# Optimization experiments

Hardware: AMD Instinct MI355X
Metric: run time of the kernel (lower is better)

Reference implementation:

```python
import jax, jax.numpy as jnp
import numpy as np

B, NQ, C = 2, 16384, 768
NH, NL, NP = 6, 1, 4
HW = 128
D = C // NH  # 128, deform_ratio = 1.0
EPS = 1e-6


def layernorm(x, g, b):
    m = jnp.mean(x, -1, keepdims=True)
    v = jnp.var(x, -1, keepdims=True)
    return (x - m) * jax.lax.rsqrt(v + EPS) * g + b


def setup_inputs() -> dict:
    key = jax.random.key(0)
    ks = jax.random.split(key, 16)
    n = lambda k, s, sc=1.0: jax.random.normal(k, s, jnp.float32) * sc
    return {
        "query": n(ks[0], (B, NQ, C)),
        "reference_points": jax.random.uniform(ks[1], (B, NQ, NL, 2), jnp.float32),
        "feat": n(ks[2], (B, NQ, C)),
        "spatial_shapes": jnp.array([[HW, HW]], jnp.int32),
        "level_start_index": jnp.array([0], jnp.int32),
        "qn_g": jnp.ones((C,), jnp.float32), "qn_b": jnp.zeros((C,), jnp.float32),
        "fn_g": jnp.ones((C,), jnp.float32), "fn_b": jnp.zeros((C,), jnp.float32),
        "gamma": n(ks[3], (C,), 0.1),
        "W_off": n(ks[4], (C, NH * NL * NP * 2), 0.02), "b_off": n(ks[5], (NH * NL * NP * 2,), 0.5),
        "W_attn": n(ks[6], (C, NH * NL * NP), 0.02), "b_attn": jnp.zeros((NH * NL * NP,), jnp.float32),
        "W_val": n(ks[7], (C, NH * D), 0.02), "b_val": jnp.zeros((NH * D,), jnp.float32),
        "W_out": n(ks[8], (NH * D, C), 0.02), "b_out": jnp.zeros((C,), jnp.float32),
    }


def _ms_deform_attn(q, rp, f, W_off, b_off, W_attn, b_attn, W_val, b_val, W_out, b_out, shapes, starts):
    Bq, Nq, _ = q.shape
    value = (f @ W_val + b_val).reshape(Bq, -1, NH, D)  # (B, Lin, H, D)
    off = (q @ W_off + b_off).reshape(Bq, Nq, NH, NL, NP, 2)
    aw = jax.nn.softmax((q @ W_attn + b_attn).reshape(Bq, Nq, NH, NL * NP), -1)
    aw = aw.reshape(Bq, Nq, NH, NL, NP)
    shapes_f = jnp.asarray(shapes, q.dtype)
    normalizer = jnp.stack([shapes_f[:, 1], shapes_f[:, 0]], -1)  # (NL, 2) = (W, H)
    loc = rp[:, :, None, :, None, :] + off / normalizer[None, None, None, :, None, :]
    out = jnp.zeros((Bq, Nq, NH, D), q.dtype)
    b_idx = jnp.arange(Bq)[:, None, None, None]
    h_idx = jnp.arange(NH)[None, None, :, None]
    for l in range(NL):
        Hl, Wl = int(shapes[l, 0]), int(shapes[l, 1])
        s = int(starts[l])
        v = value[:, s:s + Hl * Wl].reshape(Bq, Hl, Wl, NH, D)
        ll = loc[:, :, :, l]                        # (B, Nq, H, P, 2)
        # grid_sample bilinear, align_corners=False, zero padding
        x = ll[..., 0] * Wl - 0.5
        y = ll[..., 1] * Hl - 0.5
        x0 = jnp.floor(x); y0 = jnp.floor(y)
        x1 = x0 + 1.0;     y1 = y0 + 1.0
        wx1 = x - x0; wx0 = 1.0 - wx1
        wy1 = y - y0; wy0 = 1.0 - wy1
        def corner(xi, yi, w):
            valid = (xi >= 0) & (xi <= Wl - 1) & (yi >= 0) & (yi <= Hl - 1)
            xc = jnp.clip(xi, 0, Wl - 1).astype(jnp.int32)
            yc = jnp.clip(yi, 0, Hl - 1).astype(jnp.int32)
            g = v[b_idx, yc, xc, h_idx]             # (B, Nq, H, P, D)
            return g * (w * valid)[..., None]
        samp = (corner(x0, y0, wx0 * wy0) + corner(x1, y0, wx1 * wy0)
                + corner(x0, y1, wx0 * wy1) + corner(x1, y1, wx1 * wy1))
        out = out + jnp.einsum('bqhpd,bqhp->bqhd', samp, aw[:, :, :, l])
    return out.reshape(Bq, Nq, NH * D) @ W_out + b_out


def reference(query, reference_points, feat, spatial_shapes, level_start_index,
              qn_g, qn_b, fn_g, fn_b, gamma,
              W_off, b_off, W_attn, b_attn, W_val, b_val, W_out, b_out):
    shapes = np.asarray(spatial_shapes)
    starts = np.asarray(level_start_index)
    q = layernorm(query, qn_g, qn_b)
    f = layernorm(feat, fn_g, fn_b)
    attn = _ms_deform_attn(q, reference_points, f, W_off, b_off, W_attn, b_attn,
                           W_val, b_val, W_out, b_out, shapes, starts)
    return query + gamma * attn
```

## Files before the change

### kernel.cpp

```cpp
#include <hip/hip_runtime.h>
#include <stdint.h>

typedef unsigned short u16;
typedef float f32x4 __attribute__((ext_vector_type(4)));
typedef short s16x8 __attribute__((ext_vector_type(8)));

#define K_DIM 768
#define M_ROWS 32768
#define NQ_ 16384
#define HW_ 128

__device__ __forceinline__ float bf2f(u16 u) {
    union { uint32_t u; float f; } c; c.u = ((uint32_t)u) << 16; return c.f;
}
__device__ __forceinline__ u16 f2bf(float f) {
    union { float f; uint32_t u; } c; c.f = f;
    uint32_t u = c.u;
    u += 0x7FFFu + ((u >> 16) & 1);
    return (u16)(u >> 16);
}

__device__ __forceinline__ void gload_lds16(const void* g, void* l) {
    __builtin_amdgcn_global_load_lds((const __attribute__((address_space(1))) void*)g,
                                     (__attribute__((address_space(3))) void*)l, 16, 0, 0);
}

__global__ void prep_all_kernel(const float* __restrict__ Wval, const float* __restrict__ Wout,
                                const float* __restrict__ Woff, const float* __restrict__ Wattn,
                                const float* __restrict__ boff, const float* __restrict__ battn,
                                u16* __restrict__ wv_t, u16* __restrict__ wo_t,
                                u16* __restrict__ woa_t, float* __restrict__ bias) {
    int idx = blockIdx.x * 256 + threadIdx.x;
    const int SZ = 768 * K_DIM;
    if (idx < SZ) {
        int n = idx / K_DIM, k = idx - n * K_DIM;
        wv_t[idx] = f2bf(Wval[(size_t)k * 768 + n]);
    } else if (idx < 2 * SZ) {
        int r = idx - SZ;
        int n = r / K_DIM, k = r - n * K_DIM;
        wo_t[r] = f2bf(Wout[(size_t)k * 768 + n]);
    } else if (idx < 2 * SZ + 128 * K_DIM) {
        int r = idx - 2 * SZ;
        int n = r / K_DIM, k = r - n * K_DIM;
        float v = 0.0f;
        if (n < 48)      v = Woff[(size_t)k * 48 + n];
        else if (n < 72) v = Wattn[(size_t)k * 24 + (n - 48)];
        woa_t[r] = f2bf(v);
        if (r < 128) bias[r] = r < 48 ? boff[r] : (r < 72 ? battn[r - 48] : 0.0f);
    }
}

__global__ __launch_bounds__(192) void ln_kernel(const float* __restrict__ x,
                                                 const float* __restrict__ g,
                                                 const float* __restrict__ b,
                                                 u16* __restrict__ out) {
    int row = blockIdx.x;
    int tid = threadIdx.x;
    const float4 v = ((const float4*)(x + (size_t)row * K_DIM))[tid];
    float s  = v.x + v.y + v.z + v.w;
    float s2 = v.x * v.x + v.y * v.y + v.z * v.z + v.w * v.w;
#pragma unroll
    for (int off = 32; off >= 1; off >>= 1) {
        s  += __shfl_down(s, off);
        s2 += __shfl_down(s2, off);
    }
    __shared__ float red[6];
    int wv = tid >> 6, lane = tid & 63;
    if (lane == 0) { red[wv] = s; red[3 + wv] = s2; }
    __syncthreads();
    s  = red[0] + red[1] + red[2];
    s2 = red[3] + red[4] + red[5];
    float mean = s * (1.0f / K_DIM);
    float var  = s2 * (1.0f / K_DIM) - mean * mean;
    float inv  = rsqrtf(var + 1e-6f);
    const float4 gg = ((const float4*)g)[tid];
    const float4 bb = ((const float4*)b)[tid];
    ushort4 o;
    o.x = f2bf((v.x - mean) * inv * gg.x + bb.x);
    o.y = f2bf((v.y - mean) * inv * gg.y + bb.y);
    o.z = f2bf((v.z - mean) * inv * gg.z + bb.z);
    o.w = f2bf((v.w - mean) * inv * gg.w + bb.w);
    ((ushort4*)(out + (size_t)row * K_DIM))[tid] = o;
}

#define EP_BF16 0
#define EP_F32 1
#define EP_FINAL 2

template <int EP, int NX, int BN = 128>
__global__ __launch_bounds__(512) void gemm_kernel(
        const u16* __restrict__ A, const u16* __restrict__ Bt,
        const float* __restrict__ bias, void* __restrict__ out, int ld_out,
        const float* __restrict__ query, const float* __restrict__ gamma) {
    constexpr int NF = BN / 64;
    constexpr int BCH = BN / 64;
    constexpr int BUF = 16384 + BN * 128;
    constexpr int NWG = NX * (M_ROWS / 128);
    constexpr int CPX = NWG / 8;
    __shared__ __align__(16) char smem[2 * BUF];
    const int lane = threadIdx.x & 63;
    const int wv = threadIdx.x >> 6;
    const int wr = wv >> 2, wc = wv & 3;
    const int lr = lane & 15, lg = lane >> 4;
    const int wg  = blockIdx.x;
    const int swz = (wg & 7) * CPX + (wg >> 3);
    const int m0 = (swz / NX) * 128;
    const int n0 = (swz % NX) * BN;

    f32x4 acc[4][NF] = {};

    const u16* Ab = A + (size_t)m0 * K_DIM;
    const u16* Bb = Bt + (size_t)n0 * K_DIM;

    auto stage = [&](char* buf, int kt) {
#pragma unroll
        for (int c = 0; c < 2; ++c) {
            int chunk = wv * 2 + c;
            int row = chunk * 8 + (lane >> 3);
            int slot = (lane & 7) ^ (row & 7);
            gload_lds16(Ab + (size_t)row * K_DIM + kt + slot * 8, buf + chunk * 1024);
        }
#pragma unroll
        for (int c = 0; c < BCH; ++c) {
            int chunk = wv * BCH + c;
            int row = chunk * 8 + (lane >> 3);
            int slot = (lane & 7) ^ (row & 7);
            gload_lds16(Bb + (size_t)row * K_DIM + kt + slot * 8, buf + 16384 + chunk * 1024);
        }
    };

    stage(smem, 0);
    asm volatile("s_waitcnt vmcnt(0)" ::: "memory");
    __builtin_amdgcn_s_barrier();
    __builtin_amdgcn_sched_barrier(0);

    constexpr int NT = K_DIM / 64;
    int cur = 0;
#pragma unroll 2
    for (int t = 0; t < NT; ++t) {
        const char* rb = smem + cur * BUF;
        if (t + 1 < NT) stage(smem + (cur ^ 1) * BUF, (t + 1) * 64);
#pragma unroll
        for (int kk = 0; kk < 2; ++kk) {
            s16x8 af[4], bfr[NF];
#pragma unroll
            for (int m = 0; m < 4; ++m) {
                int row = wr * 64 + m * 16 + lr;
                int slot = (kk * 4 + lg) ^ (row & 7);
                af[m] = *(const s16x8*)(rb + row * 128 + slot * 16);
            }
#pragma unroll
            for (int n = 0; n < NF; ++n) {
                int row = wc * (BN / 4) + n * 16 + lr;
                int slot = (kk * 4 + lg) ^ (row & 7);
                bfr[n] = *(const s16x8*)(rb + 16384 + row * 128 + slot * 16);
            }
            __builtin_amdgcn_s_setprio(1);
#pragma unroll
            for (int m = 0; m < 4; ++m)
#pragma unroll
                for (int n = 0; n < NF; ++n)
                    acc[m][n] = __builtin_amdgcn_mfma_f32_16x16x32_bf16(af[m], bfr[n], acc[m][n], 0, 0, 0);
            __builtin_amdgcn_s_setprio(0);
        }
        asm volatile("s_waitcnt vmcnt(0)" ::: "memory");
        __builtin_amdgcn_s_barrier();
        __builtin_amdgcn_sched_barrier(0);
        cur ^= 1;
    }

#pragma unroll
    for (int m = 0; m < 4; ++m) {
#pragma unroll
        for (int r = 0; r < 4; ++r) {
            int row = m0 + wr * 64 + m * 16 + lg * 4 + r;
#pragma unroll
            for (int n = 0; n < NF; ++n) {
                int col = n0 + wc * (BN / 4) + n * 16 + lr;
                float v = acc[m][n][r] + bias[col];
                if constexpr (EP == EP_BF16) {
                    ((u16*)out)[(size_t)row * ld_out + col] = f2bf(v);
                } else if constexpr (EP == EP_F32) {
                    if (col < 72)
                        ((float*)out)[(size_t)row * ld_out + col] = v;
                } else {
                    size_t idx = (size_t)row * ld_out + col;
                    ((float*)out)[idx] = query[idx] + gamma[col] * v;
                }
            }
        }
    }
}

__global__ __launch_bounds__(384) void sample_kernel(
        const float* __restrict__ oa,
        const float* __restrict__ rp,
        const u16* __restrict__ value,
        u16* __restrict__ samp) {
    const int q = blockIdx.x;
    const int h = __builtin_amdgcn_readfirstlane(threadIdx.x >> 6);
    const int lane = threadIdx.x & 63;
    const int b = q >> 14;
    const float* oar = oa + (size_t)q * 128;

    const int p  = (lane >> 2) & 3;
    const int cn = lane & 3;
    const float lp = oar[48 + h * 4 + p];
    const float e  = __expf(lp);
    float es = e;
    es += __shfl_xor(es, 4);
    es += __shfl_xor(es, 8);
    const float aw = e * __builtin_amdgcn_rcpf(es);

    const float2 offv = *(const float2*)(oar + h * 8 + p * 2);
    const float2 rpv  = *(const float2*)(rp + (size_t)q * 2);
    const float xx = rpv.x * 128.0f + offv.x - 0.5f;
    const float yy = rpv.y * 128.0f + offv.y - 0.5f;
    const float x0 = floorf(xx), y0 = floorf(yy);
    const float fx = xx - x0, fy = yy - y0;
    const float cx = x0 + (float)(cn & 1);
    const float cy = y0 + (float)(cn >> 1);
    const float wx = (cn & 1) ? fx : 1.0f - fx;
    const float wy = (cn >> 1) ? fy : 1.0f - fy;
    const bool valid = (cx >= 0.0f) & (cx <= 127.0f) & (cy >= 0.0f) & (cy <= 127.0f);
    const float w = valid ? aw * wx * wy : 0.0f;
    const int cxi = (int)fminf(fmaxf(cx, 0.0f), 127.0f);
    const int cyi = (int)fminf(fmaxf(cy, 0.0f), 127.0f);
    const int ofs = (cyi * HW_ + cxi) * (K_DIM * 2);

    const char* vbs = (const char*)value + 2u * ((size_t)b * NQ_ * K_DIM + (size_t)h * 128);
    const int wbits = __float_as_int(w);
    float acc0 = 0.0f, acc1 = 0.0f;
#pragma unroll
    for (int c = 0; c < 16; ++c) {
        const float wc = __int_as_float(__builtin_amdgcn_readlane(wbits, c));
        const int   oc = __builtin_amdgcn_readlane(ofs, c);
        const uint32_t d = ((const uint32_t*)(vbs + oc))[lane];
        acc0 = fmaf(wc, __int_as_float(d << 16), acc0);
        acc1 = fmaf(wc, __int_as_float(d & 0xffff0000u), acc1);
    }
    ushort2 o; o.x = f2bf(acc0); o.y = f2bf(acc1);
    ((ushort2*)(samp + (size_t)q * K_DIM + h * 128))[lane] = o;
}

extern "C" void kernel_launch(void* const* d_in, const int* in_sizes, int n_in,
                              void* d_out, int out_size, void* d_ws, size_t ws_size,
                              hipStream_t stream) {
    (void)in_sizes; (void)n_in; (void)out_size; (void)ws_size;
    const float* query  = (const float*)d_in[0];
    const float* rp     = (const float*)d_in[1];
    const float* feat   = (const float*)d_in[2];
    const float* qn_g   = (const float*)d_in[5];
    const float* qn_b   = (const float*)d_in[6];
    const float* fn_g   = (const float*)d_in[7];
    const float* fn_b   = (const float*)d_in[8];
    const float* gamma  = (const float*)d_in[9];
    const float* W_off  = (const float*)d_in[10];
    const float* b_off  = (const float*)d_in[11];
    const float* W_attn = (const float*)d_in[12];
    const float* b_attn = (const float*)d_in[13];
    const float* W_val  = (const float*)d_in[14];
    const float* b_val  = (const float*)d_in[15];
    const float* W_out  = (const float*)d_in[16];
    const float* b_out  = (const float*)d_in[17];

    char* ws = (char*)d_ws;
    u16*   ln_buf  = (u16*)  (ws + 0);
    u16*   val_buf = (u16*)  (ws + 50331648);
    float* oa_buf  = (float*)(ws + 100663296);
    u16*   wv_t    = (u16*)  (ws + 117440512);
    u16*   wo_t    = (u16*)  (ws + 118620160);
    u16*   woa_t   = (u16*)  (ws + 119799808);
    float* bias_oa = (float*)(ws + 119996416);
    u16*   samp_buf = ln_buf;

    prep_all_kernel<<<(2 * 768 * 768 + 128 * 768 + 255) / 256, 256, 0, stream>>>(
        W_val, W_out, W_off, W_attn, b_off, b_attn, wv_t, wo_t, woa_t, bias_oa);

    ln_kernel<<<M_ROWS, 192, 0, stream>>>(feat, fn_g, fn_b, ln_buf);

    gemm_kernel<EP_BF16, 6><<<6 * (M_ROWS / 128), 512, 0, stream>>>(ln_buf, wv_t, b_val, val_buf, 768, nullptr, nullptr);

    ln_kernel<<<M_ROWS, 192, 0, stream>>>(query, qn_g, qn_b, ln_buf);

    gemm_kernel<EP_F32, 2, 64><<<2 * (M_ROWS / 128), 512, 0, stream>>>(ln_buf, woa_t, bias_oa, oa_buf, 128, nullptr, nullptr);

    sample_kernel<<<M_ROWS, 384, 0, stream>>>(oa_buf, rp, val_buf, samp_buf);

    gemm_kernel<EP_FINAL, 6><<<6 * (M_ROWS / 128), 512, 0, stream>>>(samp_buf, wo_t, b_out, d_out, 768, query, gamma);
}
```

Baseline: 258.7 us.

## Triple-buffer A tiles and restructure GEMM K-loop for deeper prefetch

```diff
diff --git a/kernel.cpp b/kernel.cpp
--- a/kernel.cpp
+++ b/kernel.cpp
@@ -92,12 +92,14 @@
         const u16* __restrict__ A, const u16* __restrict__ Bt,
         const float* __restrict__ bias, void* __restrict__ out, int ld_out,
         const float* __restrict__ query, const float* __restrict__ gamma) {
-    constexpr int NF = BN / 64;
+    constexpr int NF  = BN / 64;
     constexpr int BCH = BN / 64;
-    constexpr int BUF = 16384 + BN * 128;
+    constexpr int ASZ = 16384;
+    constexpr int BSZ = BN * 128;
     constexpr int NWG = NX * (M_ROWS / 128);
     constexpr int CPX = NWG / 8;
-    __shared__ __align__(16) char smem[2 * BUF];
+    __shared__ __align__(16) char asmem[3 * ASZ];
+    __shared__ __align__(16) char bsmem[2 * BSZ];
     const int lane = threadIdx.x & 63;
     const int wv = threadIdx.x >> 6;
     const int wr = wv >> 2, wc = wv & 3;
@@ -112,7 +114,7 @@
     const u16* Ab = A + (size_t)m0 * K_DIM;
     const u16* Bb = Bt + (size_t)n0 * K_DIM;
 
-    auto stage = [&](char* buf, int kt) {
+    auto stageA = [&](char* buf, int kt) {
 #pragma unroll
         for (int c = 0; c < 2; ++c) {
             int chunk = wv * 2 + c;
@@ -120,26 +122,17 @@
             int slot = (lane & 7) ^ (row & 7);
             gload_lds16(Ab + (size_t)row * K_DIM + kt + slot * 8, buf + chunk * 1024);
         }
+    };
+    auto stageB = [&](char* buf, int kt) {
 #pragma unroll
         for (int c = 0; c < BCH; ++c) {
             int chunk = wv * BCH + c;
             int row = chunk * 8 + (lane >> 3);
             int slot = (lane & 7) ^ (row & 7);
-            gload_lds16(Bb + (size_t)row * K_DIM + kt + slot * 8, buf + 16384 + chunk * 1024);
+            gload_lds16(Bb + (size_t)row * K_DIM + kt + slot * 8, buf + chunk * 1024);
         }
     };
-
-    stage(smem, 0);
-    asm volatile("s_waitcnt vmcnt(0)" ::: "memory");
-    __builtin_amdgcn_s_barrier();
-    __builtin_amdgcn_sched_barrier(0);
-
-    constexpr int NT = K_DIM / 64;
-    int cur = 0;
-#pragma unroll 2
-    for (int t = 0; t < NT; ++t) {
-        const char* rb = smem + cur * BUF;
-        if (t + 1 < NT) stage(smem + (cur ^ 1) * BUF, (t + 1) * 64);
+    auto compute = [&](const char* ra, const char* rbuf) {
 #pragma unroll
         for (int kk = 0; kk < 2; ++kk) {
             s16x8 af[4], bfr[NF];
@@ -147,13 +140,13 @@
             for (int m = 0; m < 4; ++m) {
                 int row = wr * 64 + m * 16 + lr;
                 int slot = (kk * 4 + lg) ^ (row & 7);
-                af[m] = *(const s16x8*)(rb + row * 128 + slot * 16);
+                af[m] = *(const s16x8*)(ra + row * 128 + slot * 16);
             }
 #pragma unroll
             for (int n = 0; n < NF; ++n) {
                 int row = wc * (BN / 4) + n * 16 + lr;
                 int slot = (kk * 4 + lg) ^ (row & 7);
-                bfr[n] = *(const s16x8*)(rb + 16384 + row * 128 + slot * 16);
+                bfr[n] = *(const s16x8*)(rbuf + row * 128 + slot * 16);
             }
             __builtin_amdgcn_s_setprio(1);
 #pragma unroll
@@ -163,11 +156,27 @@
                     acc[m][n] = __builtin_amdgcn_mfma_f32_16x16x32_bf16(af[m], bfr[n], acc[m][n], 0, 0, 0);
             __builtin_amdgcn_s_setprio(0);
         }
-        asm volatile("s_waitcnt vmcnt(0)" ::: "memory");
+    };
+
+    constexpr int NT = K_DIM / 64;
+    stageA(asmem, 0);
+    stageB(bsmem, 0);
+    stageA(asmem + ASZ, 64);
+
+#pragma unroll
+    for (int t = 0; t < NT - 1; ++t) {
+        asm volatile("s_waitcnt vmcnt(2)" ::: "memory");
         __builtin_amdgcn_s_barrier();
         __builtin_amdgcn_sched_barrier(0);
-        cur ^= 1;
-    }
+        stageB(bsmem + ((t + 1) & 1) * BSZ, (t + 1) * 64);
+        if (t + 2 < NT) stageA(asmem + ((t + 2) % 3) * ASZ, (t + 2) * 64);
+        __builtin_amdgcn_sched_barrier(0);
+        compute(asmem + (t % 3) * ASZ, bsmem + (t & 1) * BSZ);
+    }
+    asm volatile("s_waitcnt vmcnt(0)" ::: "memory");
+    __builtin_amdgcn_s_barrier();
+    __builtin_amdgcn_sched_barrier(0);
+    compute(asmem + ((NT - 1) % 3) * ASZ, bsmem + ((NT - 1) & 1) * BSZ);
 
 #pragma unroll
     for (int m = 0; m < 4; ++m) {
```

Result: slower. 266.5 us (+3.0%).
